# Optimization experiments

Measured on AMD Instinct MI355X. Metric: run time of the kernel, lower is better.

## Reference

```python
import jax, jax.numpy as jnp
import numpy as np

N_PATHS, N_LINKS, L, DEG, D = 50000, 10000, 8, 40, 64
ITERS = 8
# (min, scale) pairs from override_min_max_scores
MM_FT = (0.0, 1e-4); MM_FP = (0.0, 1e-3); MM_FPS = (0.0, 1e-3); MM_LC = (0.0, 1e-5)


def _gru(x, h, wx, wh, bx, bh):
    # Keras GRUCell (reset_after=True, tanh/sigmoid)
    mx = x @ wx + bx
    mh = h @ wh + bh
    xz, xr, xh = jnp.split(mx, 3, axis=-1)
    rz, rr, rh = jnp.split(mh, 3, axis=-1)
    z = jax.nn.sigmoid(xz + rz)
    r = jax.nn.sigmoid(xr + rr)
    hh = jnp.tanh(xh + r * rh)
    return z * h + (1.0 - z) * hh


def setup_inputs():
    key = jax.random.key(0)
    ks = jax.random.split(key, 30)
    w = lambda k, s: jax.random.normal(k, s, jnp.float32) * 0.05
    inp = {
        'flow_traffic': jax.random.uniform(ks[0], (N_PATHS, 1), jnp.float32, 100.0, 10000.0),
        'flow_packets': jax.random.uniform(ks[1], (N_PATHS, 1), jnp.float32, 1.0, 1000.0),
        'flow_packet_size': jax.random.uniform(ks[2], (N_PATHS, 1), jnp.float32, 100.0, 1500.0),
        'link_capacity': jax.random.uniform(ks[3], (N_LINKS, 1), jnp.float32, 1.0, 100.0),
        'link_to_path': jax.random.randint(ks[4], (N_PATHS, L), 0, N_LINKS, jnp.int32),
        'path_to_link': jnp.stack([
            jax.random.randint(ks[5], (N_LINKS, DEG), 0, N_PATHS, jnp.int32),
            jax.random.randint(ks[6], (N_LINKS, DEG), 1, L + 1, jnp.int32)], axis=-1),
        'pe_w1': w(ks[7], (3, D)), 'pe_b1': jnp.zeros((D,), jnp.float32),
        'pe_w2': w(ks[8], (D, D)), 'pe_b2': jnp.zeros((D,), jnp.float32),
        'le_w1': w(ks[9], (2, D)), 'le_b1': jnp.zeros((D,), jnp.float32),
        'le_w2': w(ks[10], (D, D)), 'le_b2': jnp.zeros((D,), jnp.float32),
        'pg_wx': w(ks[11], (D, 3 * D)), 'pg_wh': w(ks[12], (D, 3 * D)),
        'pg_bx': jnp.zeros((3 * D,), jnp.float32), 'pg_bh': jnp.zeros((3 * D,), jnp.float32),
        'lg_wx': w(ks[13], (D, 3 * D)), 'lg_wh': w(ks[14], (D, 3 * D)),
        'lg_bx': jnp.zeros((3 * D,), jnp.float32), 'lg_bh': jnp.zeros((3 * D,), jnp.float32),
        'ro_w1': w(ks[15], (D, D // 2)), 'ro_b1': jnp.zeros((D // 2,), jnp.float32),
        'ro_w2': w(ks[16], (D // 2, D // 4)), 'ro_b2': jnp.zeros((D // 4,), jnp.float32),
        'ro_w3': w(ks[17], (D // 4, 1)), 'ro_b3': jnp.zeros((1,), jnp.float32),
    }
    return inp


def reference(flow_traffic, flow_packets, flow_packet_size, link_capacity, link_to_path, path_to_link,
              pe_w1, pe_b1, pe_w2, pe_b2, le_w1, le_b1, le_w2, le_b2,
              pg_wx, pg_wh, pg_bx, pg_bh, lg_wx, lg_wh, lg_bx, lg_bh,
              ro_w1, ro_b1, ro_w2, ro_b2, ro_w3, ro_b3):
    # per-link load: sum of traffic of paths crossing the link / capacity
    load = flow_traffic[path_to_link[:, :, 0], 0].sum(axis=1, keepdims=True) / (link_capacity * 1e9)
    # initial embeddings (min-max scaled features)
    pe_in = jnp.concatenate([(flow_traffic - MM_FT[0]) * MM_FT[1],
                             (flow_packets - MM_FP[0]) * MM_FP[1],
                             (flow_packet_size - MM_FPS[0]) * MM_FPS[1]], axis=1)
    path_state = jax.nn.relu(jax.nn.relu(pe_in @ pe_w1 + pe_b1) @ pe_w2 + pe_b2)  # [n_paths, D]
    le_in = jnp.concatenate([(link_capacity - MM_LC[0]) * MM_LC[1], load], axis=1)
    link_state = jax.nn.relu(jax.nn.relu(le_in @ le_w1 + le_b1) @ le_w2 + le_b2)  # [n_links, D]

    path_state_sequence = None
    for _ in range(ITERS):
        link_gather = link_state[link_to_path]  # [n_paths, L, D]
        prev = path_state

        def step(h, x_t):
            h2 = _gru(x_t, h, pg_wx, pg_wh, pg_bx, pg_bh)
            return h2, h2

        path_state, seq = jax.lax.scan(step, path_state, jnp.swapaxes(link_gather, 0, 1))
        path_state_sequence = jnp.concatenate([prev[:, None], jnp.swapaxes(seq, 0, 1)], axis=1)  # [n_paths, L+1, D]
        # gather_nd over (path index, position in path) then sum per link
        path_gather = path_state_sequence[path_to_link[:, :, 0], path_to_link[:, :, 1]]  # [n_links, DEG, D]
        path_sum = path_gather.sum(axis=1)  # [n_links, D]
        link_state = _gru(path_sum, link_state, lg_wx, lg_wh, lg_bx, lg_bh)

    h = jax.nn.relu(path_state_sequence[:, 1:] @ ro_w1 + ro_b1)
    h = jax.nn.relu(h @ ro_w2 + ro_b2)
    occupancy = jax.nn.softplus(h @ ro_w3 + ro_b3)  # [n_paths, L, 1]
    capacity_gather = link_capacity[link_to_path]  # [n_paths, L, 1]
    delay = (occupancy / capacity_gather).sum(axis=1)  # [n_paths, 1]
    return delay
```

## Files before the change

### kernel.cpp

```cpp
#include <hip/hip_runtime.h>
#include <math.h>

#define N_PATHS 50000
#define N_LINKS 10000
#define LPATH   8
#define DEG     40
#define DIM     64
#define G3      192
#define ITERS   8

typedef float f32x4  __attribute__((ext_vector_type(4)));
typedef short bf16x8 __attribute__((ext_vector_type(8)));

__device__ __forceinline__ float fsigmoid(float x){ return 1.0f/(1.0f + __expf(-x)); }
__device__ __forceinline__ float ftanh(float x){ return 1.0f - 2.0f/(__expf(2.0f*x) + 1.0f); }
__device__ __forceinline__ unsigned short bf16_rne(float v){
  unsigned u = __float_as_uint(v);
  return (unsigned short)((u + 0x7FFFu + ((u>>16)&1u)) >> 16);
}
__device__ __forceinline__ unsigned pack_bf16(float a, float b){
  unsigned r;
  asm("v_cvt_pk_bf16_f32 %0, %1, %2" : "=v"(r) : "v"(a), "v"(b));
  return r;
}
__device__ __forceinline__ float lo16f(unsigned v){ return __uint_as_float(v << 16); }
__device__ __forceinline__ float hi16f(unsigned v){ return __uint_as_float(v & 0xFFFF0000u); }
__device__ __forceinline__ void split8(const float* s, bf16x8& hi, bf16x8& lo){
  #pragma unroll
  for (int e=0;e<8;e++){
    unsigned short hb = bf16_rne(s[e]);
    float lof = s[e] - __uint_as_float(((unsigned)hb)<<16);
    hi[e] = (short)hb; lo[e] = (short)bf16_rne(lof);
  }
}
__device__ __forceinline__ void accum8(float* a, uint4 v){
  unsigned x[4] = {v.x, v.y, v.z, v.w};
  #pragma unroll
  for (int q=0;q<4;q++){
    a[2*q]   += __uint_as_float((x[q]&0xFFFFu)<<16);
    a[2*q+1] += __uint_as_float(x[q]&0xFFFF0000u);
  }
}

__global__ __launch_bounds__(256) void path_embed(
    const float* __restrict__ ft, const float* __restrict__ fp, const float* __restrict__ fps,
    const float* __restrict__ w1, const float* __restrict__ b1,
    const float* __restrict__ w2, const float* __restrict__ b2,
    float* __restrict__ path_state)
{
  __shared__ float h1[4][DIM];
  int j  = threadIdx.x & 63;
  int pl = threadIdx.x >> 6;
  int p  = blockIdx.x*4 + pl;
  float x0 = ft[p]*1e-4f, x1 = fp[p]*1e-3f, x2 = fps[p]*1e-3f;
  float h = b1[j] + x0*w1[0*DIM+j] + x1*w1[1*DIM+j] + x2*w1[2*DIM+j];
  h1[pl][j] = fmaxf(h, 0.f);
  __syncthreads();
  float acc = b2[j];
  #pragma unroll 8
  for (int k=0;k<DIM;k++) acc = fmaf(h1[pl][k], w2[k*DIM+j], acc);
  path_state[p*DIM+j] = fmaxf(acc, 0.f);
}

__global__ __launch_bounds__(256) void link_embed(
    const float* __restrict__ ft, const float* __restrict__ cap, const int* __restrict__ ptl,
    const float* __restrict__ w1, const float* __restrict__ b1,
    const float* __restrict__ w2, const float* __restrict__ b2,
    float* __restrict__ link_state)
{
  __shared__ float h1[4][DIM];
  int j  = threadIdx.x & 63;
  int wl = threadIdx.x >> 6;
  int l  = blockIdx.x*4 + wl;
  float s = 0.f;
  if (j < DEG) s = ft[ptl[(l*DEG + j)*2 + 0]];
  #pragma unroll
  for (int off=32; off; off>>=1) s += __shfl_down(s, off);
  float load = __shfl(s, 0) / (cap[l]*1e9f);
  float x0 = cap[l]*1e-5f;
  float h = b1[j] + x0*w1[0*DIM+j] + load*w1[1*DIM+j];
  h1[wl][j] = fmaxf(h, 0.f);
  __syncthreads();
  float acc = b2[j];
  #pragma unroll 8
  for (int k=0;k<DIM;k++) acc = fmaf(h1[wl][k], w2[k*DIM+j], acc);
  link_state[l*DIM+j] = fmaxf(acc, 0.f);
}

__global__ __launch_bounds__(256) void pack_frags(
    const float* __restrict__ pg_wh, const float* __restrict__ pg_wx,
    const float* __restrict__ lg_wx, const float* __restrict__ lg_wh,
    unsigned short* __restrict__ whf)
{
  int tid = blockIdx.x*256 + threadIdx.x;
  if (tid >= 4*24*512) return;
  int i = tid & 7, l = (tid>>3)&63, f = (tid>>9)%24, m = tid/(24*512);
  int nt = f>>1, kc = f&1;
  int k = kc*32 + (l>>4)*8 + i;
  int n = nt*16 + (l&15);
  const float* src = (m==0)?pg_wh : (m==1)?pg_wx : (m==2)?lg_wx : lg_wh;
  whf[tid] = bf16_rne(src[k*G3 + n]);
}

__global__ __launch_bounds__(192) void compute_lx(
    const float* __restrict__ link_state, const float* __restrict__ wx,
    const float* __restrict__ bx, const float* __restrict__ bh,
    unsigned short* __restrict__ LXq)
{
  __shared__ float ls[4][DIM];
  int g  = threadIdx.x;
  int l0 = blockIdx.x*4;
  if (g < DIM){
    #pragma unroll
    for (int li=0; li<4; li++) ls[li][g] = link_state[(l0+li)*DIM+g];
  }
  __syncthreads();
  float b = bx[g] + (g < 128 ? bh[g] : 0.f);
  float a0=b, a1=b, a2=b, a3=b;
  #pragma unroll 8
  for (int k=0;k<DIM;k++){
    float w = wx[k*G3+g];
    a0 = fmaf(ls[0][k], w, a0);
    a1 = fmaf(ls[1][k], w, a1);
    a2 = fmaf(ls[2][k], w, a2);
    a3 = fmaf(ls[3][k], w, a3);
  }
  int comp = g >> 6, dim = g & 63;
  int pos = dim*3 + comp;
  LXq[(size_t)(l0+0)*G3+pos]=bf16_rne(a0);
  LXq[(size_t)(l0+1)*G3+pos]=bf16_rne(a1);
  LXq[(size_t)(l0+2)*G3+pos]=bf16_rne(a2);
  LXq[(size_t)(l0+3)*G3+pos]=bf16_rne(a3);
}

__global__ __launch_bounds__(256) void path_scan_mfma(
    const unsigned short* __restrict__ LXq, const int* __restrict__ ltp,
    const unsigned short* __restrict__ whf, const float* __restrict__ bh,
    float* __restrict__ path_state, unsigned short* __restrict__ seq16)
{
  __shared__ __align__(16) unsigned short htile[2][16*72];
  __shared__ int ltps[128];
  int tid = threadIdx.x, l = tid & 63, w = tid >> 6;
  int lg = l >> 4, lr = l & 15;
  int p0 = blockIdx.x*16;

  bf16x8 bf[3][2];
  #pragma unroll
  for (int j=0;j<3;j++){
    int nt = w + j*4;
    bf[j][0] = *(const bf16x8*)(whf + (size_t)(nt*2+0)*512 + l*8);
    bf[j][1] = *(const bf16x8*)(whf + (size_t)(nt*2+1)*512 + l*8);
  }
  float bhq[4];
  #pragma unroll
  for (int r=0;r<4;r++) bhq[r] = bh[128 + w*16 + lg*4 + r];

  if (tid < 128) ltps[tid] = ltp[(size_t)p0*LPATH + tid];

  {
    int pi = tid >> 4, c4 = (tid & 15)*4;
    float4 v = *(const float4*)(path_state + (size_t)(p0+pi)*DIM + c4);
    uint2 u = make_uint2(pack_bf16(v.x, v.y), pack_bf16(v.z, v.w));
    *(uint2*)&htile[0][pi*72 + c4] = u;
  }
  f32x4 hold = *(const f32x4*)(path_state + (size_t)(p0+lr)*DIM + w*16 + lg*4);

  __syncthreads();

  unsigned short* seqp = seq16 + ((size_t)(p0+lr)*LPATH)*DIM + w*16 + lg*4;
  const size_t dimoff = (size_t)(w*16 + lg*4)*3;
  int cur = 0;

  uint2 c0, c1, c2;
  {
    const unsigned short* x = LXq + (size_t)ltps[lr*LPATH]*G3 + dimoff;
    c0 = *(const uint2*)x; c1 = *(const uint2*)(x+4); c2 = *(const uint2*)(x+8);
  }

  for (int t=0; t<LPATH; t++){
    int tn = (t < LPATH-1) ? t+1 : t;
    const unsigned short* xn = LXq + (size_t)ltps[lr*LPATH + tn]*G3 + dimoff;
    uint2 n0 = *(const uint2*)xn, n1 = *(const uint2*)(xn+4), n2 = *(const uint2*)(xn+8);

    bf16x8 h0 = *(const bf16x8*)&htile[cur][lr*72 +  0 + lg*8];
    bf16x8 h1 = *(const bf16x8*)&htile[cur][lr*72 + 32 + lg*8];
    f32x4 accz = (f32x4){0.f,0.f,0.f,0.f};
    f32x4 accr = (f32x4){0.f,0.f,0.f,0.f};
    f32x4 accq = (f32x4){bhq[0],bhq[1],bhq[2],bhq[3]};
    accz = __builtin_amdgcn_mfma_f32_16x16x32_bf16(bf[0][0], h0, accz, 0,0,0);
    accr = __builtin_amdgcn_mfma_f32_16x16x32_bf16(bf[1][0], h0, accr, 0,0,0);
    accq = __builtin_amdgcn_mfma_f32_16x16x32_bf16(bf[2][0], h0, accq, 0,0,0);
    accz = __builtin_amdgcn_mfma_f32_16x16x32_bf16(bf[0][1], h1, accz, 0,0,0);
    accr = __builtin_amdgcn_mfma_f32_16x16x32_bf16(bf[1][1], h1, accr, 0,0,0);
    accq = __builtin_amdgcn_mfma_f32_16x16x32_bf16(bf[2][1], h1, accq, 0,0,0);

    float lz[4]  = { lo16f(c0.x), hi16f(c0.y), lo16f(c1.y), hi16f(c2.x) };
    float lrr[4] = { hi16f(c0.x), lo16f(c1.x), hi16f(c1.y), lo16f(c2.y) };
    float lq[4]  = { lo16f(c0.y), hi16f(c1.x), lo16f(c2.x), hi16f(c2.y) };
    f32x4 hn;
    #pragma unroll
    for (int r=0;r<4;r++){
      float z  = fsigmoid(lz[r]  + accz[r]);
      float rr = fsigmoid(lrr[r] + accr[r]);
      float hh = ftanh(lq[r] + rr*accq[r]);
      hn[r] = z*hold[r] + (1.f-z)*hh;
    }
    hold = hn;
    uint2 u = make_uint2(pack_bf16(hn[0], hn[1]), pack_bf16(hn[2], hn[3]));
    *(uint2*)&htile[cur^1][lr*72 + w*16 + lg*4] = u;
    *(uint2*)(seqp + (size_t)t*DIM) = u;
    __syncthreads();
    cur ^= 1;
    c0 = n0; c1 = n1; c2 = n2;
  }
  *(f32x4*)(path_state + (size_t)(p0+lr)*DIM + w*16 + lg*4) = hold;
}

__global__ __launch_bounds__(256) void link_fused(
    const unsigned short* __restrict__ seq16, const int* __restrict__ ptl,
    const unsigned short* __restrict__ whf,
    const float* __restrict__ lbx, const float* __restrict__ lbh,
    const float* __restrict__ pbx, const float* __restrict__ pbh,
    float* __restrict__ link_state, unsigned short* __restrict__ LXq)
{
  __shared__ float pspart[4][16][64];
  __shared__ float tile[16*68];
  int tid = threadIdx.x, l = tid & 63, w = tid >> 6;
  int lr = l & 15, lg = l >> 4;
  int l0 = blockIdx.x*16;

  float ps[16];
  #pragma unroll
  for (int i=0;i<16;i++) ps[i]=0.f;
  {
    const int* pe = ptl + (size_t)(l0+lr)*DEG*2 + w*10*2;
    #pragma unroll
    for (int d=0; d<10; d++){
      int pp = pe[2*d], tt = pe[2*d+1];
      const unsigned short* rowp = seq16 + ((size_t)pp*LPATH + (tt-1))*DIM;
      accum8(ps,   *(const uint4*)(rowp + lg*8));
      accum8(ps+8, *(const uint4*)(rowp + 32 + lg*8));
    }
  }
  #pragma unroll
  for (int i=0;i<16;i++) pspart[w][i][l] = ps[i];
  __syncthreads();

  #pragma unroll
  for (int i=0;i<16;i++)
    ps[i] = pspart[0][i][l] + pspart[1][i][l] + pspart[2][i][l] + pspart[3][i][l];

  bf16x8 phi[2], plo[2], lhi[2], llo[2];
  #pragma unroll
  for (int kc=0;kc<2;kc++){
    split8(ps + kc*8, phi[kc], plo[kc]);
    float hs[8];
    const float* lsr = link_state + (size_t)(l0+lr)*DIM + kc*32 + lg*8;
    *(f32x4*)hs = *(const f32x4*)lsr;
    *(f32x4*)(hs+4) = *(const f32x4*)(lsr+4);
    split8(hs, lhi[kc], llo[kc]);
  }
  f32x4 mxa[3], mha[3];
  #pragma unroll
  for (int j=0;j<3;j++){
    int nt = w + j*4;
    float bxv = lbx[nt*16+lr], bhv = lbh[nt*16+lr];
    mxa[j] = (f32x4){bxv,bxv,bxv,bxv};
    mha[j] = (f32x4){bhv,bhv,bhv,bhv};
    #pragma unroll
    for (int kc=0;kc<2;kc++){
      bf16x8 bwx = *(const bf16x8*)(whf + (size_t)((2*24 + nt*2+kc)*512) + l*8);
      mxa[j] = __builtin_amdgcn_mfma_f32_16x16x32_bf16(phi[kc], bwx, mxa[j], 0,0,0);
      mxa[j] = __builtin_amdgcn_mfma_f32_16x16x32_bf16(plo[kc], bwx, mxa[j], 0,0,0);
      bf16x8 bwh = *(const bf16x8*)(whf + (size_t)((3*24 + nt*2+kc)*512) + l*8);
      mha[j] = __builtin_amdgcn_mfma_f32_16x16x32_bf16(lhi[kc], bwh, mha[j], 0,0,0);
      mha[j] = __builtin_amdgcn_mfma_f32_16x16x32_bf16(llo[kc], bwh, mha[j], 0,0,0);
    }
  }
  __syncthreads();

  #pragma unroll
  for (int r=0;r<4;r++){
    size_t lk = (size_t)(l0 + lg*4 + r)*DIM + w*16 + lr;
    float lsv = link_state[lk];
    float z  = fsigmoid(mxa[0][r] + mha[0][r]);
    float rr = fsigmoid(mxa[1][r] + mha[1][r]);
    float hh = ftanh(mxa[2][r] + rr*mha[2][r]);
    float hn = z*lsv + (1.f-z)*hh;
    link_state[lk] = hn;
    tile[(lg*4+r)*68 + w*16 + lr] = hn;
  }
  __syncthreads();

  f32x4 lxa[3];
  #pragma unroll
  for (int j=0;j<3;j++){
    int g = (w + j*4)*16 + lr;
    float b = pbx[g] + (g < 128 ? pbh[g] : 0.f);
    lxa[j] = (f32x4){b,b,b,b};
  }
  #pragma unroll
  for (int kc=0;kc<2;kc++){
    float hs[8];
    #pragma unroll
    for (int i=0;i<8;i++) hs[i] = tile[lr*68 + kc*32 + lg*8 + i];
    bf16x8 thi, tlo; split8(hs, thi, tlo);
    #pragma unroll
    for (int j=0;j<3;j++){
      int nt = w + j*4;
      bf16x8 bw = *(const bf16x8*)(whf + (size_t)((1*24 + nt*2+kc)*512) + l*8);
      lxa[j] = __builtin_amdgcn_mfma_f32_16x16x32_bf16(thi, bw, lxa[j], 0,0,0);
      lxa[j] = __builtin_amdgcn_mfma_f32_16x16x32_bf16(tlo, bw, lxa[j], 0,0,0);
    }
  }
  #pragma unroll
  for (int r=0;r<4;r++){
    int link = l0 + lg*4 + r;
    size_t base = (size_t)link*G3 + (size_t)(w*16 + lr)*3;
    LXq[base+0] = bf16_rne(lxa[0][r]);
    LXq[base+1] = bf16_rne(lxa[1][r]);
    LXq[base+2] = bf16_rne(lxa[2][r]);
  }
}

__global__ __launch_bounds__(256) void readout(
    const unsigned short* __restrict__ seq16, const int* __restrict__ ltp,
    const float* __restrict__ cap,
    const float* __restrict__ w1, const float* __restrict__ b1,
    const float* __restrict__ w2, const float* __restrict__ b2,
    const float* __restrict__ w3, const float* __restrict__ b3,
    float* __restrict__ out)
{
  __shared__ unsigned short rows_sh[4][64*72];
  __shared__ float w1s[DIM*32];
  __shared__ float w2s[32*16];
  __shared__ float w3s[16];
  __shared__ float b1s[32], b2s[16];
  int tid = threadIdx.x;
  for (int i=tid;i<DIM*32;i+=256) w1s[i]=w1[i];
  for (int i=tid;i<32*16;i+=256) w2s[i]=w2[i];
  if (tid<16) w3s[tid]=w3[tid];
  if (tid<32) b1s[tid]=b1[tid];
  if (tid<16) b2s[tid]=b2[tid];
  __syncthreads();

  int l = tid & 63, w = tid >> 6;
  size_t wave_r = (size_t)blockIdx.x*256 + (size_t)w*64;
  if (wave_r >= (size_t)N_PATHS*LPATH) return;

  const unsigned short* src = seq16 + wave_r*DIM;
  #pragma unroll
  for (int i=0;i<16;i++){
    int e  = i*64 + l;
    int ri = e >> 4;
    int c4 = e & 15;
    *(uint2*)&rows_sh[w][ri*72 + c4*4] = *(const uint2*)(src + (size_t)e*4);
  }

  size_t row = wave_r + l;
  const unsigned short* myrow = &rows_sh[w][l*72];
  float a[32];
  #pragma unroll
  for (int j=0;j<32;j++) a[j]=b1s[j];
  #pragma unroll
  for (int c=0;c<16;c++){
    uint2 v = *(const uint2*)(myrow + c*4);
    float f0 = __uint_as_float((v.x & 0xFFFFu) << 16);
    float f1 = __uint_as_float(v.x & 0xFFFF0000u);
    float f2 = __uint_as_float((v.y & 0xFFFFu) << 16);
    float f3 = __uint_as_float(v.y & 0xFFFF0000u);
    #pragma unroll
    for (int j=0;j<32;j++) a[j] = fmaf(f0, w1s[(c*4+0)*32+j], a[j]);
    #pragma unroll
    for (int j=0;j<32;j++) a[j] = fmaf(f1, w1s[(c*4+1)*32+j], a[j]);
    #pragma unroll
    for (int j=0;j<32;j++) a[j] = fmaf(f2, w1s[(c*4+2)*32+j], a[j]);
    #pragma unroll
    for (int j=0;j<32;j++) a[j] = fmaf(f3, w1s[(c*4+3)*32+j], a[j]);
  }
  float h2[16];
  #pragma unroll
  for (int j2=0;j2<16;j2++) h2[j2]=b2s[j2];
  #pragma unroll
  for (int j=0;j<32;j++){
    float hv = fmaxf(a[j],0.f);
    #pragma unroll
    for (int j2=0;j2<16;j2++) h2[j2] = fmaf(hv, w2s[j*16+j2], h2[j2]);
  }
  float o = b3[0];
  #pragma unroll
  for (int j2=0;j2<16;j2++) o = fmaf(fmaxf(h2[j2],0.f), w3s[j2], o);
  float sp = (o > 20.f) ? o : log1pf(__expf(o));
  float dly = sp / cap[ltp[row]];
  dly += __shfl_xor(dly, 1);
  dly += __shfl_xor(dly, 2);
  dly += __shfl_xor(dly, 4);
  if ((l & 7) == 0) out[row >> 3] = dly;
}

extern "C" void kernel_launch(void* const* d_in, const int* in_sizes, int n_in,
                              void* d_out, int out_size, void* d_ws, size_t ws_size,
                              hipStream_t stream) {
  const float* ft    = (const float*)d_in[0];
  const float* fpk   = (const float*)d_in[1];
  const float* fps   = (const float*)d_in[2];
  const float* cap   = (const float*)d_in[3];
  const int*   ltp   = (const int*)  d_in[4];
  const int*   ptl   = (const int*)  d_in[5];
  const float* pe_w1 = (const float*)d_in[6];
  const float* pe_b1 = (const float*)d_in[7];
  const float* pe_w2 = (const float*)d_in[8];
  const float* pe_b2 = (const float*)d_in[9];
  const float* le_w1 = (const float*)d_in[10];
  const float* le_b1 = (const float*)d_in[11];
  const float* le_w2 = (const float*)d_in[12];
  const float* le_b2 = (const float*)d_in[13];
  const float* pg_wx = (const float*)d_in[14];
  const float* pg_wh = (const float*)d_in[15];
  const float* pg_bx = (const float*)d_in[16];
  const float* pg_bh = (const float*)d_in[17];
  const float* lg_wx = (const float*)d_in[18];
  const float* lg_wh = (const float*)d_in[19];
  const float* lg_bx = (const float*)d_in[20];
  const float* lg_bh = (const float*)d_in[21];
  const float* ro_w1 = (const float*)d_in[22];
  const float* ro_b1 = (const float*)d_in[23];
  const float* ro_w2 = (const float*)d_in[24];
  const float* ro_b2 = (const float*)d_in[25];
  const float* ro_w3 = (const float*)d_in[26];
  const float* ro_b3 = (const float*)d_in[27];
  float* out = (float*)d_out;

  float* path_state = (float*)d_ws;
  float* link_state = path_state + (size_t)N_PATHS*DIM;
  unsigned short* LXq   = (unsigned short*)(link_state + (size_t)N_LINKS*DIM);
  unsigned short* seq16 = LXq + (size_t)N_LINKS*G3;
  unsigned short* whf   = seq16 + (size_t)N_PATHS*LPATH*DIM;

  path_embed<<<N_PATHS/4, 256, 0, stream>>>(ft, fpk, fps, pe_w1, pe_b1, pe_w2, pe_b2, path_state);
  link_embed<<<N_LINKS/4, 256, 0, stream>>>(ft, cap, ptl, le_w1, le_b1, le_w2, le_b2, link_state);
  pack_frags<<<192, 256, 0, stream>>>(pg_wh, pg_wx, lg_wx, lg_wh, whf);
  compute_lx<<<N_LINKS/4, 192, 0, stream>>>(link_state, pg_wx, pg_bx, pg_bh, LXq);
  for (int it=0; it<ITERS; ++it){
    path_scan_mfma<<<N_PATHS/16, 256, 0, stream>>>(LXq, ltp, whf, pg_bh, path_state, seq16);
    if (it < ITERS-1)
      link_fused<<<N_LINKS/16, 256, 0, stream>>>(seq16, ptl, whf,
          lg_bx, lg_bh, pg_bx, pg_bh, link_state, LXq);
  }
  readout<<<(N_PATHS*LPATH + 255)/256, 256, 0, stream>>>(seq16, ltp, cap,
      ro_w1, ro_b1, ro_w2, ro_b2, ro_w3, ro_b3, out);
}
```

Measured before the change: 633.8 us.

## Give each wavefront its own 16-path GRU scan and drop per-step block barriers

The path GRU scan kernel now assigns 16 paths to each wavefront (64 paths per block) instead of splitting one 16-path tile's gate columns across four waves. Each wave computes all 12 MFMA output tiles itself, reading recurrent weight fragments from LDS that the block stages once. Because the hidden-state tile is private to the wave, the per-timestep __syncthreads is removed. The trade-off is more LDS traffic for weights, more accumulator registers per thread, and fewer blocks. The last block clamps its start index, so some paths are computed twice with identical results.

```diff
diff --git a/kernel.cpp b/kernel.cpp
--- a/kernel.cpp
+++ b/kernel.cpp
@@ -8,6 +8,7 @@
 #define DIM     64
 #define G3      192
 #define ITERS   8
+#define HP      76
 
 typedef float f32x4  __attribute__((ext_vector_type(4)));
 typedef short bf16x8 __attribute__((ext_vector_type(8)));
@@ -138,82 +139,80 @@
     const unsigned short* __restrict__ whf, const float* __restrict__ bh,
     float* __restrict__ path_state, unsigned short* __restrict__ seq16)
 {
-  __shared__ __align__(16) unsigned short htile[2][16*72];
-  __shared__ int ltps[128];
+  __shared__ __align__(16) unsigned short bw_lds[24*512];
+  __shared__ __align__(16) unsigned short htile[4][16*HP];
+  __shared__ float bq_lds[DIM];
+  __shared__ int ltps[4][128];
   int tid = threadIdx.x, l = tid & 63, w = tid >> 6;
   int lg = l >> 4, lr = l & 15;
-  int p0 = blockIdx.x*16;
-
-  bf16x8 bf[3][2];
-  #pragma unroll
-  for (int j=0;j<3;j++){
-    int nt = w + j*4;
-    bf[j][0] = *(const bf16x8*)(whf + (size_t)(nt*2+0)*512 + l*8);
-    bf[j][1] = *(const bf16x8*)(whf + (size_t)(nt*2+1)*512 + l*8);
-  }
-  float bhq[4];
-  #pragma unroll
-  for (int r=0;r<4;r++) bhq[r] = bh[128 + w*16 + lg*4 + r];
-
-  if (tid < 128) ltps[tid] = ltp[(size_t)p0*LPATH + tid];
-
-  {
-    int pi = tid >> 4, c4 = (tid & 15)*4;
-    float4 v = *(const float4*)(path_state + (size_t)(p0+pi)*DIM + c4);
-    uint2 u = make_uint2(pack_bf16(v.x, v.y), pack_bf16(v.z, v.w));
-    *(uint2*)&htile[0][pi*72 + c4] = u;
-  }
-  f32x4 hold = *(const f32x4*)(path_state + (size_t)(p0+lr)*DIM + w*16 + lg*4);
-
-  __syncthreads();
-
-  unsigned short* seqp = seq16 + ((size_t)(p0+lr)*LPATH)*DIM + w*16 + lg*4;
-  const size_t dimoff = (size_t)(w*16 + lg*4)*3;
-  int cur = 0;
-
-  uint2 c0, c1, c2;
-  {
-    const unsigned short* x = LXq + (size_t)ltps[lr*LPATH]*G3 + dimoff;
-    c0 = *(const uint2*)x; c1 = *(const uint2*)(x+4); c2 = *(const uint2*)(x+8);
-  }
+  int p0 = blockIdx.x*64 + w*16;
+  if (p0 > N_PATHS-16) p0 = N_PATHS-16;
+
+  { const uint4* src=(const uint4*)whf; uint4* dst=(uint4*)bw_lds;
+    #pragma unroll
+    for (int i=0;i<6;i++) dst[i*256+tid] = src[i*256+tid]; }
+  if (tid < DIM) bq_lds[tid] = bh[128 + tid];
+
+  *(int2*)&ltps[w][l*2] = *(const int2*)(ltp + (size_t)p0*LPATH + l*2);
+
+  f32x4 hold[4];
+  #pragma unroll
+  for (int t4=0;t4<4;t4++){
+    hold[t4] = *(const f32x4*)(path_state + (size_t)(p0+lr)*DIM + t4*16 + lg*4);
+    uint2 u = make_uint2(pack_bf16(hold[t4][0], hold[t4][1]), pack_bf16(hold[t4][2], hold[t4][3]));
+    *(uint2*)&htile[w][lr*HP + t4*16 + lg*4] = u;
+  }
+
+  __syncthreads();
+
+  unsigned short* seqp = seq16 + ((size_t)(p0+lr)*LPATH)*DIM;
 
   for (int t=0; t<LPATH; t++){
-    int tn = (t < LPATH-1) ? t+1 : t;
-    const unsigned short* xn = LXq + (size_t)ltps[lr*LPATH + tn]*G3 + dimoff;
-    uint2 n0 = *(const uint2*)xn, n1 = *(const uint2*)(xn+4), n2 = *(const uint2*)(xn+8);
-
-    bf16x8 h0 = *(const bf16x8*)&htile[cur][lr*72 +  0 + lg*8];
-    bf16x8 h1 = *(const bf16x8*)&htile[cur][lr*72 + 32 + lg*8];
-    f32x4 accz = (f32x4){0.f,0.f,0.f,0.f};
-    f32x4 accr = (f32x4){0.f,0.f,0.f,0.f};
-    f32x4 accq = (f32x4){bhq[0],bhq[1],bhq[2],bhq[3]};
-    accz = __builtin_amdgcn_mfma_f32_16x16x32_bf16(bf[0][0], h0, accz, 0,0,0);
-    accr = __builtin_amdgcn_mfma_f32_16x16x32_bf16(bf[1][0], h0, accr, 0,0,0);
-    accq = __builtin_amdgcn_mfma_f32_16x16x32_bf16(bf[2][0], h0, accq, 0,0,0);
-    accz = __builtin_amdgcn_mfma_f32_16x16x32_bf16(bf[0][1], h1, accz, 0,0,0);
-    accr = __builtin_amdgcn_mfma_f32_16x16x32_bf16(bf[1][1], h1, accr, 0,0,0);
-    accq = __builtin_amdgcn_mfma_f32_16x16x32_bf16(bf[2][1], h1, accq, 0,0,0);
-
-    float lz[4]  = { lo16f(c0.x), hi16f(c0.y), lo16f(c1.y), hi16f(c2.x) };
-    float lrr[4] = { hi16f(c0.x), lo16f(c1.x), hi16f(c1.y), lo16f(c2.y) };
-    float lq[4]  = { lo16f(c0.y), hi16f(c1.x), lo16f(c2.x), hi16f(c2.y) };
-    f32x4 hn;
-    #pragma unroll
-    for (int r=0;r<4;r++){
-      float z  = fsigmoid(lz[r]  + accz[r]);
-      float rr = fsigmoid(lrr[r] + accr[r]);
-      float hh = ftanh(lq[r] + rr*accq[r]);
-      hn[r] = z*hold[r] + (1.f-z)*hh;
-    }
-    hold = hn;
-    uint2 u = make_uint2(pack_bf16(hn[0], hn[1]), pack_bf16(hn[2], hn[3]));
-    *(uint2*)&htile[cur^1][lr*72 + w*16 + lg*4] = u;
-    *(uint2*)(seqp + (size_t)t*DIM) = u;
-    __syncthreads();
-    cur ^= 1;
-    c0 = n0; c1 = n1; c2 = n2;
-  }
-  *(f32x4*)(path_state + (size_t)(p0+lr)*DIM + w*16 + lg*4) = hold;
+    int lk = ltps[w][lr*LPATH + t];
+    const unsigned short* lx = LXq + (size_t)lk*G3;
+    uint2 xa[4][3];
+    #pragma unroll
+    for (int t4=0;t4<4;t4++){
+      #pragma unroll
+      for (int jj=0;jj<3;jj++)
+        xa[t4][jj] = *(const uint2*)(lx + t4*48 + lg*12 + jj*4);
+    }
+    bf16x8 h0 = *(const bf16x8*)&htile[w][lr*HP +  0 + lg*8];
+    bf16x8 h1 = *(const bf16x8*)&htile[w][lr*HP + 32 + lg*8];
+    f32x4 acc[12];
+    #pragma unroll
+    for (int nt=0;nt<8;nt++) acc[nt] = (f32x4){0.f,0.f,0.f,0.f};
+    #pragma unroll
+    for (int t4=0;t4<4;t4++) acc[8+t4] = *(const f32x4*)&bq_lds[t4*16 + lg*4];
+    #pragma unroll
+    for (int nt=0;nt<12;nt++){
+      bf16x8 w0 = *(const bf16x8*)&bw_lds[(nt*2+0)*512 + l*8];
+      acc[nt] = __builtin_amdgcn_mfma_f32_16x16x32_bf16(w0, h0, acc[nt], 0,0,0);
+      bf16x8 w1 = *(const bf16x8*)&bw_lds[(nt*2+1)*512 + l*8];
+      acc[nt] = __builtin_amdgcn_mfma_f32_16x16x32_bf16(w1, h1, acc[nt], 0,0,0);
+    }
+    #pragma unroll
+    for (int t4=0;t4<4;t4++){
+      float lz[4]  = { lo16f(xa[t4][0].x), hi16f(xa[t4][0].y), lo16f(xa[t4][1].y), hi16f(xa[t4][2].x) };
+      float lrr[4] = { hi16f(xa[t4][0].x), lo16f(xa[t4][1].x), hi16f(xa[t4][1].y), lo16f(xa[t4][2].y) };
+      float lq[4]  = { lo16f(xa[t4][0].y), hi16f(xa[t4][1].x), lo16f(xa[t4][2].x), hi16f(xa[t4][2].y) };
+      f32x4 hn;
+      #pragma unroll
+      for (int r=0;r<4;r++){
+        float z  = fsigmoid(lz[r]  + acc[t4][r]);
+        float rr = fsigmoid(lrr[r] + acc[4+t4][r]);
+        float hh = ftanh(lq[r] + rr*acc[8+t4][r]);
+        hn[r] = z*hold[t4][r] + (1.f-z)*hh;
+      }
+      hold[t4] = hn;
+      uint2 u = make_uint2(pack_bf16(hn[0], hn[1]), pack_bf16(hn[2], hn[3]));
+      *(uint2*)&htile[w][lr*HP + t4*16 + lg*4] = u;
+      *(uint2*)(seqp + (size_t)t*DIM + t4*16 + lg*4) = u;
+    }
+  }
+  #pragma unroll
+  for (int t4=0;t4<4;t4++)
+    *(f32x4*)(path_state + (size_t)(p0+lr)*DIM + t4*16 + lg*4) = hold[t4];
 }
 
 __global__ __launch_bounds__(256) void link_fused(
@@ -442,7 +441,7 @@
   pack_frags<<<192, 256, 0, stream>>>(pg_wh, pg_wx, lg_wx, lg_wh, whf);
   compute_lx<<<N_LINKS/4, 192, 0, stream>>>(link_state, pg_wx, pg_bx, pg_bh, LXq);
   for (int it=0; it<ITERS; ++it){
-    path_scan_mfma<<<N_PATHS/16, 256, 0, stream>>>(LXq, ltp, whf, pg_bh, path_state, seq16);
+    path_scan_mfma<<<(N_PATHS+63)/64, 256, 0, stream>>>(LXq, ltp, whf, pg_bh, path_state, seq16);
     if (it < ITERS-1)
       link_fused<<<N_LINKS/16, 256, 0, stream>>>(seq16, ptl, whf,
           lg_bx, lg_bh, pg_bx, pg_bh, link_state, LXq);
```

Result: slower. 752.4 us (+18.7%).

## Stage gathered link projections through double-buffered LDS with coalesced row loads

Applied to the files above, without the earlier changes.

The path scan kernel no longer has each lane fetch three scattered 8-byte chunks of the gathered link-input row. Each wave now loads whole 384-byte rows for 4 paths with 16-byte loads (24 lanes per row) into a double-buffered shared tile, and lanes read their slice from LDS. The per-step __syncthreads is replaced by an explicit lgkmcnt wait plus s_barrier with sched barriers. This aims for more coalesced global gathers, at the cost of extra LDS traffic, more shared memory per block and idle lanes during the loads.

```diff
diff --git a/kernel.cpp b/kernel.cpp
--- a/kernel.cpp
+++ b/kernel.cpp
@@ -8,6 +8,7 @@
 #define DIM     64
 #define G3      192
 #define ITERS   8
+#define LXP     200
 
 typedef float f32x4  __attribute__((ext_vector_type(4)));
 typedef short bf16x8 __attribute__((ext_vector_type(8)));
@@ -138,6 +139,7 @@
     const unsigned short* __restrict__ whf, const float* __restrict__ bh,
     float* __restrict__ path_state, unsigned short* __restrict__ seq16)
 {
+  __shared__ __align__(16) unsigned short lxb[2][16*LXP];
   __shared__ __align__(16) unsigned short htile[2][16*72];
   __shared__ int ltps[128];
   int tid = threadIdx.x, l = tid & 63, w = tid >> 6;
@@ -167,20 +169,32 @@
 
   __syncthreads();
 
+  {
+    #pragma unroll
+    for (int i=0;i<4;i++){
+      int row = w*4 + i;
+      int lk = ltps[row*LPATH + 0];
+      if (l < 24){
+        uint4 v = *(const uint4*)(LXq + (size_t)lk*G3 + l*8);
+        *(uint4*)&lxb[0][row*LXP + l*8] = v;
+      }
+    }
+  }
+  __syncthreads();
+
   unsigned short* seqp = seq16 + ((size_t)(p0+lr)*LPATH)*DIM + w*16 + lg*4;
-  const size_t dimoff = (size_t)(w*16 + lg*4)*3;
+  const int lxoff = w*48 + lg*12;
   int cur = 0;
-
-  uint2 c0, c1, c2;
-  {
-    const unsigned short* x = LXq + (size_t)ltps[lr*LPATH]*G3 + dimoff;
-    c0 = *(const uint2*)x; c1 = *(const uint2*)(x+4); c2 = *(const uint2*)(x+8);
-  }
 
   for (int t=0; t<LPATH; t++){
     int tn = (t < LPATH-1) ? t+1 : t;
-    const unsigned short* xn = LXq + (size_t)ltps[lr*LPATH + tn]*G3 + dimoff;
-    uint2 n0 = *(const uint2*)xn, n1 = *(const uint2*)(xn+4), n2 = *(const uint2*)(xn+8);
+    uint4 ld[4];
+    #pragma unroll
+    for (int i=0;i<4;i++){
+      int lk = ltps[(w*4+i)*LPATH + tn];
+      if (l < 24) ld[i] = *(const uint4*)(LXq + (size_t)lk*G3 + l*8);
+    }
+    __builtin_amdgcn_sched_barrier(0);
 
     bf16x8 h0 = *(const bf16x8*)&htile[cur][lr*72 +  0 + lg*8];
     bf16x8 h1 = *(const bf16x8*)&htile[cur][lr*72 + 32 + lg*8];
@@ -194,6 +208,10 @@
     accr = __builtin_amdgcn_mfma_f32_16x16x32_bf16(bf[1][1], h1, accr, 0,0,0);
     accq = __builtin_amdgcn_mfma_f32_16x16x32_bf16(bf[2][1], h1, accq, 0,0,0);
 
+    const unsigned short* myx = &lxb[cur][lr*LXP + lxoff];
+    uint2 c0 = *(const uint2*)(myx);
+    uint2 c1 = *(const uint2*)(myx+4);
+    uint2 c2 = *(const uint2*)(myx+8);
     float lz[4]  = { lo16f(c0.x), hi16f(c0.y), lo16f(c1.y), hi16f(c2.x) };
     float lrr[4] = { hi16f(c0.x), lo16f(c1.x), hi16f(c1.y), lo16f(c2.y) };
     float lq[4]  = { lo16f(c0.y), hi16f(c1.x), lo16f(c2.x), hi16f(c2.y) };
@@ -209,9 +227,19 @@
     uint2 u = make_uint2(pack_bf16(hn[0], hn[1]), pack_bf16(hn[2], hn[3]));
     *(uint2*)&htile[cur^1][lr*72 + w*16 + lg*4] = u;
     *(uint2*)(seqp + (size_t)t*DIM) = u;
-    __syncthreads();
+
+    #pragma unroll
+    for (int i=0;i<4;i++){
+      if (l < 24)
+        *(uint4*)&lxb[cur^1][(w*4+i)*LXP + l*8] = ld[i];
+    }
+
+    __builtin_amdgcn_sched_barrier(0);
+    asm volatile("s_waitcnt lgkmcnt(0)" ::: "memory");
+    __builtin_amdgcn_s_barrier();
+    __builtin_amdgcn_sched_barrier(0);
+
     cur ^= 1;
-    c0 = n0; c1 = n1; c2 = n2;
   }
   *(f32x4*)(path_state + (size_t)(p0+lr)*DIM + w*16 + lg*4) = hold;
 }
```

New measurement: 905.3 us. 42.8% more time.
